# Kernel optimization log

Measured on AMD Instinct MI355X. Metric: run time of the kernel, lower is better.

Reference implementation:

```python
import jax, jax.numpy as jnp
import numpy as np

B, L, H, NH, NB = 8, 200, 128, 4, 2
HD = H // NH
ITEM_NUM, TIME_SPAN = 50000, 256
PAD = -2.0**32 + 1.0


def setup_inputs() -> dict:
    key = jax.random.key(0)
    ks = jax.random.split(key, 32)
    def g(i, shape, s=0.02):
        return jax.random.normal(ks[i], shape, jnp.float32) * s
    item_emb = g(0, (ITEM_NUM + 1, H)).at[0].set(0.0)  # padding_idx=0
    return dict(
        user_ids=jax.random.randint(ks[1], (B,), 0, 1000),
        log_seqs=jax.random.randint(ks[2], (B, L), 0, ITEM_NUM),
        time_matrices=jax.random.randint(ks[3], (B, L, L), 0, TIME_SPAN + 1),
        pos_seqs=jax.random.randint(ks[4], (B, L), 0, ITEM_NUM + 1),
        neg_seqs=jax.random.randint(ks[5], (B, L), 0, ITEM_NUM + 1),
        item_emb=item_emb,
        pos_K_emb=g(6, (L, H)), pos_V_emb=g(7, (L, H)),
        time_K_emb=g(8, (TIME_SPAN + 1, H)), time_V_emb=g(9, (TIME_SPAN + 1, H)),
        attn_ln_g=jnp.ones((NB, H)), attn_ln_b=jnp.zeros((NB, H)),
        Wq=g(10, (NB, H, H)), bq=jnp.zeros((NB, H)),
        Wk=g(11, (NB, H, H)), bk=jnp.zeros((NB, H)),
        Wv=g(12, (NB, H, H)), bv=jnp.zeros((NB, H)),
        fwd_ln_g=jnp.ones((NB, H)), fwd_ln_b=jnp.zeros((NB, H)),
        W1=g(13, (NB, H, H)), b1=jnp.zeros((NB, H)),
        W2=g(14, (NB, H, H)), b2=jnp.zeros((NB, H)),
        last_ln_g=jnp.ones((H,)), last_ln_b=jnp.zeros((H,)),
    )


def _ln(x, g, b, eps=1e-8):
    m = x.mean(-1, keepdims=True)
    v = jnp.var(x, axis=-1, keepdims=True)
    return (x - m) / jnp.sqrt(v + eps) * g + b


def _heads(x):
    # [..., H] -> [NH, ..., HD]; matches torch.cat(torch.split(x, HD, -1), 0)
    y = x.reshape(x.shape[:-1] + (NH, HD))
    return jnp.moveaxis(y, -2, 0)


def reference(user_ids, log_seqs, time_matrices, pos_seqs, neg_seqs, item_emb,
              pos_K_emb, pos_V_emb, time_K_emb, time_V_emb,
              attn_ln_g, attn_ln_b, Wq, bq, Wk, bk, Wv, bv,
              fwd_ln_g, fwd_ln_b, W1, b1, W2, b2, last_ln_g, last_ln_b):
    # user_ids is unused in the original forward as well.
    tmask = log_seqs == 0                                  # [B,L] True = pad
    keep = (~tmask)[..., None].astype(jnp.float32)
    seqs = item_emb[log_seqs] * np.float32(np.sqrt(H))
    seqs = seqs * keep
    pKh = _heads(pos_K_emb)                                # [NH,L,HD]
    pVh = _heads(pos_V_emb)
    tKh = _heads(time_K_emb[time_matrices])                # [NH,B,L,L,HD]
    tVh = _heads(time_V_emb[time_matrices])
    causal = ~jnp.tril(jnp.ones((L, L), bool))             # True above diag -> masked
    bad = tmask[:, :, None] | causal[None]                 # [B,L,L]
    scale = np.float32(np.sqrt(HD))
    for i in range(NB):
        Qin = _ln(seqs, attn_ln_g[i], attn_ln_b[i])
        Qh = _heads(Qin @ Wq[i].T + bq[i])                 # [NH,B,L,HD]
        Kh = _heads(seqs @ Wk[i].T + bk[i])
        Vh = _heads(seqs @ Wv[i].T + bv[i])
        attn = (jnp.einsum('nbqd,nbkd->nbqk', Qh, Kh)
                + jnp.einsum('nbqd,nkd->nbqk', Qh, pKh)
                + jnp.einsum('nbqkd,nbqd->nbqk', tKh, Qh)) / scale
        attn = jnp.where(bad[None], PAD, attn)
        attn = jax.nn.softmax(attn, axis=-1)
        out = (jnp.einsum('nbqk,nbkd->nbqd', attn, Vh)
               + jnp.einsum('nbqk,nkd->nbqd', attn, pVh)
               + jnp.einsum('nbqk,nbqkd->nbqd', attn, tVh))
        out = jnp.moveaxis(out, 0, -2).reshape(seqs.shape)  # merge heads -> [B,L,H]
        seqs = Qin + out                                    # residual uses LN'd Q (as in source)
        seqs = _ln(seqs, fwd_ln_g[i], fwd_ln_b[i])
        ff = jax.nn.relu(seqs @ W1[i].T + b1[i]) @ W2[i].T + b2[i] + seqs
        seqs = ff * keep
    log_feats = _ln(seqs, last_ln_g, last_ln_b)
    pos_logits = (log_feats * item_emb[pos_seqs]).sum(-1)   # [B,L]
    neg_logits = (log_feats * item_emb[neg_seqs]).sum(-1)
    return pos_logits, neg_logits
```

## Files before the change

kernel.cpp:

```cpp
#include <hip/hip_runtime.h>
#include <hip/hip_bf16.h>

#define BB 8
#define LL 200
#define HH 128
#define NHEAD 4
#define HDIM 32
#define NBLK 2
#define BL (BB * LL)
#define NT 257
#define QT 8
#define NQT 25
#define SSP 208
#define KC 132
#define ASP 36
#define BSP 66
#define FSP 132

static constexpr float SQRT_H    = 11.313708498984761f;
static constexpr float INV_SCALE = 0.17677669529663687f;
static constexpr float PADV      = -4294967295.0f;

__global__ void k_qkv_gemm(const float* __restrict__ seqs_in,
                           const int* __restrict__ log_seqs,
                           const float* __restrict__ item_emb,
                           const float* __restrict__ g, const float* __restrict__ bia,
                           const float* __restrict__ Wq, const float* __restrict__ bq,
                           const float* __restrict__ Wk, const float* __restrict__ bk,
                           const float* __restrict__ Wv, const float* __restrict__ bv,
                           const float* __restrict__ posK, const float* __restrict__ posV,
                           float* __restrict__ Qin, float* __restrict__ Q,
                           float* __restrict__ K, float* __restrict__ V) {
    int mt = blockIdx.x / 6, nt = blockIdx.x % 6;
    int matsel = nt >> 1;
    int jb = (nt & 1) * 64;
    int row0 = mt * 32;
    int tid = threadIdx.x;
    __shared__ float As[128 * ASP];
    __shared__ float Bs[128 * BSP];

    {
        int r = tid >> 3, seg = tid & 7;
        int row = row0 + r;
        float4 vv[4];
        if (seqs_in) {
            #pragma unroll
            for (int i = 0; i < 4; i++)
                vv[i] = *(const float4*)(seqs_in + (size_t)row * HH + seg * 16 + i * 4);
        } else {
            int idx = log_seqs[row];
            if (idx == 0) {
                #pragma unroll
                for (int i = 0; i < 4; i++) vv[i] = make_float4(0.f, 0.f, 0.f, 0.f);
            } else {
                #pragma unroll
                for (int i = 0; i < 4; i++) {
                    float4 e = *(const float4*)(item_emb + (size_t)idx * HH + seg * 16 + i * 4);
                    vv[i] = make_float4(e.x * SQRT_H, e.y * SQRT_H, e.z * SQRT_H, e.w * SQRT_H);
                }
            }
        }
        if (matsel == 0) {
            float s = 0.f, s2 = 0.f;
            #pragma unroll
            for (int i = 0; i < 4; i++) {
                s  += vv[i].x + vv[i].y + vv[i].z + vv[i].w;
                s2 += vv[i].x * vv[i].x + vv[i].y * vv[i].y + vv[i].z * vv[i].z + vv[i].w * vv[i].w;
            }
            #pragma unroll
            for (int off = 1; off < 8; off <<= 1) {
                s  += __shfl_xor(s, off);
                s2 += __shfl_xor(s2, off);
            }
            float mean = s * (1.f / HH);
            float var  = s2 * (1.f / HH) - mean * mean;
            float inv  = 1.f / sqrtf(var + 1e-8f);
            #pragma unroll
            for (int i = 0; i < 4; i++) {
                int k = seg * 16 + i * 4;
                float4 g4 = *(const float4*)(g + k);
                float4 b4 = *(const float4*)(bia + k);
                float4 y;
                y.x = (vv[i].x - mean) * inv * g4.x + b4.x;
                y.y = (vv[i].y - mean) * inv * g4.y + b4.y;
                y.z = (vv[i].z - mean) * inv * g4.z + b4.z;
                y.w = (vv[i].w - mean) * inv * g4.w + b4.w;
                As[(k + 0) * ASP + r] = y.x;
                As[(k + 1) * ASP + r] = y.y;
                As[(k + 2) * ASP + r] = y.z;
                As[(k + 3) * ASP + r] = y.w;
                if (nt == 0) *(float4*)(Qin + (size_t)row * HH + k) = y;
            }
        } else {
            #pragma unroll
            for (int i = 0; i < 4; i++) {
                int k = seg * 16 + i * 4;
                As[(k + 0) * ASP + r] = vv[i].x;
                As[(k + 1) * ASP + r] = vv[i].y;
                As[(k + 2) * ASP + r] = vv[i].z;
                As[(k + 3) * ASP + r] = vv[i].w;
            }
        }
    }
    {
        const float* W = (matsel == 0) ? Wq : (matsel == 1) ? Wk : Wv;
        int k4 = tid & 31, jj0 = tid >> 5;
        #pragma unroll
        for (int p = 0; p < 8; p++) {
            int jj = jj0 + p * 8;
            float4 w = *(const float4*)(W + (size_t)(jb + jj) * HH + k4 * 4);
            Bs[(k4 * 4 + 0) * BSP + jj] = w.x;
            Bs[(k4 * 4 + 1) * BSP + jj] = w.y;
            Bs[(k4 * 4 + 2) * BSP + jj] = w.z;
            Bs[(k4 * 4 + 3) * BSP + jj] = w.w;
        }
    }
    __syncthreads();

    int my = tid >> 5, jx = tid & 31;
    float a00=0,a01=0,a10=0,a11=0,a20=0,a21=0,a30=0,a31=0;
    #pragma unroll 4
    for (int k = 0; k < HH; k++) {
        float4 a = *(const float4*)&As[k * ASP + my * 4];
        float2 b = *(const float2*)&Bs[k * BSP + jx * 2];
        a00 += a.x * b.x; a01 += a.x * b.y;
        a10 += a.y * b.x; a11 += a.y * b.y;
        a20 += a.z * b.x; a21 += a.z * b.y;
        a30 += a.w * b.x; a31 += a.w * b.y;
    }
    float accs[4][2] = {{a00,a01},{a10,a11},{a20,a21},{a30,a31}};
    int col = jb + jx * 2;
    if (matsel == 0) {
        float2 bb = *(const float2*)(bq + col);
        #pragma unroll
        for (int r = 0; r < 4; r++) {
            int row = row0 + my * 4 + r;
            float2 o = make_float2((accs[r][0] + bb.x) * INV_SCALE,
                                   (accs[r][1] + bb.y) * INV_SCALE);
            *(float2*)(Q + (size_t)row * HH + col) = o;
        }
    } else if (matsel == 1) {
        float2 bb = *(const float2*)(bk + col);
        #pragma unroll
        for (int r = 0; r < 4; r++) {
            int row = row0 + my * 4 + r;
            int l = row % LL;
            float2 pk = *(const float2*)(posK + (size_t)l * HH + col);
            *(float2*)(K + (size_t)row * HH + col) =
                make_float2(accs[r][0] + bb.x + pk.x, accs[r][1] + bb.y + pk.y);
        }
    } else {
        float2 bb = *(const float2*)(bv + col);
        #pragma unroll
        for (int r = 0; r < 4; r++) {
            int row = row0 + my * 4 + r;
            int l = row % LL;
            float2 pv = *(const float2*)(posV + (size_t)l * HH + col);
            *(float2*)(V + (size_t)row * HH + col) =
                make_float2(accs[r][0] + bb.x + pv.x, accs[r][1] + bb.y + pv.y);
        }
    }
}

__global__ void k_attn(const float* __restrict__ Q, const float* __restrict__ K,
                       const float* __restrict__ V,
                       const float* __restrict__ timeK, const float* __restrict__ timeV,
                       const int* __restrict__ tm,
                       float* __restrict__ att) {
    int bn = blockIdx.x & 31;
    int b = bn >> 2, n = bn & 3;
    int qt = (NQT - 1) - (blockIdx.x >> 5);
    int q0 = qt * QT;
    int kmax = q0 + QT - 1;
    int tid = threadIdx.x;
    int wv = tid >> 6, ln = tid & 63;

    __shared__ float Qs[QT * HDIM];
    __shared__ float KstT[HDIM * KC];
    __shared__ float DTW[QT * NT];
    __shared__ float Ssc[QT * SSP];
    __shared__ unsigned short tmst[QT * LL];
    __shared__ float Ost[QT * HDIM];

    Ost[tid] = 0.f;
    if (tid < 64) {
        int qi = tid >> 3, d4 = tid & 7;
        *(float4*)(Qs + qi * HDIM + d4 * 4) =
            *(const float4*)(Q + ((size_t)(b * LL + q0 + qi)) * HH + n * HDIM + d4 * 4);
    }
    for (int idx = tid; idx < QT * LL; idx += 256) {
        int qi = idx / LL, k = idx - qi * LL;
        tmst[idx] = (unsigned short)tm[((size_t)(b * LL + q0 + qi)) * LL + k];
    }
    __syncthreads();

    int qi_c = tid >> 5, k2 = tid & 31;

    for (int c = 0; c < 2; c++) {
        int base = c * 128, rows = c ? 129 : 128;
        #pragma unroll
        for (int p = 0; p < 5; p++) {
            int idx = tid + p * 256;
            int r = idx >> 3, d4 = idx & 7;
            if (r < rows) {
                float4 w = *(const float4*)(timeK + (size_t)(base + r) * HH + n * HDIM + d4 * 4);
                KstT[(d4 * 4 + 0) * KC + r] = w.x;
                KstT[(d4 * 4 + 1) * KC + r] = w.y;
                KstT[(d4 * 4 + 2) * KC + r] = w.z;
                KstT[(d4 * 4 + 3) * KC + r] = w.w;
            }
        }
        __syncthreads();
        float a0 = 0, a1 = 0, a2 = 0, a3 = 0;
        int col = k2 * 4;
        #pragma unroll 8
        for (int d = 0; d < HDIM; d++) {
            float qv = Qs[qi_c * HDIM + d];
            float4 kv = *(const float4*)&KstT[d * KC + col];
            a0 += qv * kv.x; a1 += qv * kv.y; a2 += qv * kv.z; a3 += qv * kv.w;
        }
        float* dt = &DTW[qi_c * NT + base + col];
        dt[0] = a0; dt[1] = a1; dt[2] = a2; dt[3] = a3;
        if (c == 1 && k2 == 0) {
            float a = 0.f;
            #pragma unroll 8
            for (int d = 0; d < HDIM; d++) a += Qs[qi_c * HDIM + d] * KstT[d * KC + 128];
            DTW[qi_c * NT + 256] = a;
        }
        __syncthreads();
    }

    int nch = (kmax >> 7) + 1;
    for (int c = 0; c < nch; c++) {
        int base = c * 128;
        int rows = min(128, kmax + 1 - base);
        #pragma unroll
        for (int p = 0; p < 4; p++) {
            int idx = tid + p * 256;
            int r = idx >> 3, d4 = idx & 7;
            if (r < rows) {
                float4 w = *(const float4*)(K + ((size_t)(b * LL + base + r)) * HH + n * HDIM + d4 * 4);
                KstT[(d4 * 4 + 0) * KC + r] = w.x;
                KstT[(d4 * 4 + 1) * KC + r] = w.y;
                KstT[(d4 * 4 + 2) * KC + r] = w.z;
                KstT[(d4 * 4 + 3) * KC + r] = w.w;
            }
        }
        __syncthreads();
        float av[4] = {0, 0, 0, 0};
        int col = k2 * 4;
        #pragma unroll 8
        for (int d = 0; d < HDIM; d++) {
            float qv = Qs[qi_c * HDIM + d];
            float4 kv = *(const float4*)&KstT[d * KC + col];
            av[0] += qv * kv.x; av[1] += qv * kv.y; av[2] += qv * kv.z; av[3] += qv * kv.w;
        }
        int q = q0 + qi_c;
        #pragma unroll
        for (int j = 0; j < 4; j++) {
            int k = base + col + j;
            if (k <= q)
                Ssc[qi_c * SSP + k] = av[j] + DTW[qi_c * NT + tmst[qi_c * LL + k]];
        }
        __syncthreads();
    }

    for (int rr = 0; rr < 2; rr++) {
        int qi = wv + rr * 4;
        int q = q0 + qi;
        float sv[4];
        float m = -3.0e38f;
        #pragma unroll
        for (int jj = 0; jj < 4; jj++) {
            int k = ln + 64 * jj;
            sv[jj] = (k <= q) ? Ssc[qi * SSP + k] : -3.0e38f;
            m = fmaxf(m, sv[jj]);
        }
        for (int off = 32; off; off >>= 1) m = fmaxf(m, __shfl_xor(m, off));
        float sum = 0.f;
        #pragma unroll
        for (int jj = 0; jj < 4; jj++) {
            int k = ln + 64 * jj;
            sv[jj] = (k <= q) ? __expf(sv[jj] - m) : 0.f;
            sum += sv[jj];
        }
        for (int off = 32; off; off >>= 1) sum += __shfl_xor(sum, off);
        float inv = 1.f / sum;
        #pragma unroll
        for (int jj = 0; jj < 4; jj++) {
            int k = ln + 64 * jj;
            if (k <= q) Ssc[qi * SSP + k] = sv[jj] * inv;
        }
    }
    __syncthreads();

    int d = tid & 31, kg = tid >> 5;
    float acc[QT] = {0,0,0,0,0,0,0,0};
    const float* vb  = V + ((size_t)(b * LL)) * HH + n * HDIM + d;
    const float* tvb = timeV + n * HDIM + d;
    for (int k = kg; k <= kmax; k += 8) {
        float v = vb[(size_t)k * HH];
        #pragma unroll
        for (int qi = 0; qi < QT; qi++) {
            if (q0 + qi >= k) {
                float tv = tvb[(size_t)tmst[qi * LL + k] * HH];
                acc[qi] += Ssc[qi * SSP + k] * (v + tv);
            }
        }
    }
    #pragma unroll
    for (int qi = 0; qi < QT; qi++) {
        acc[qi] += __shfl_xor(acc[qi], 32);
        if ((kg & 1) == 0) atomicAdd(&Ost[qi * HDIM + d], acc[qi]);
    }
    __syncthreads();
    {
        int qi = tid >> 5;
        att[((size_t)(b * LL + q0 + qi)) * HH + n * HDIM + (tid & 31)] = Ost[tid];
    }
}

__global__ void k_ffn(const float* __restrict__ Qin, const float* __restrict__ att,
                      const float* __restrict__ g, const float* __restrict__ bia,
                      const float* __restrict__ W1, const float* __restrict__ b1,
                      const float* __restrict__ W2, const float* __restrict__ b2,
                      const int* __restrict__ log_seqs,
                      const float* __restrict__ lg, const float* __restrict__ lb,
                      const float* __restrict__ item_emb,
                      const int* __restrict__ pos, const int* __restrict__ neg,
                      float* __restrict__ out, float* __restrict__ logits, int last) {
    int row0 = blockIdx.x * 4;
    int tid = threadIdx.x;
    int wv = tid >> 6, ln = tid & 63;
    __shared__ float As[4 * FSP];
    __shared__ float H1[4 * FSP];
    __shared__ float Bs[128 * BSP];

    {
        int row = row0 + wv;
        float v0 = Qin[(size_t)row * HH + ln]      + att[(size_t)row * HH + ln];
        float v1 = Qin[(size_t)row * HH + ln + 64] + att[(size_t)row * HH + ln + 64];
        float s = v0 + v1, s2 = v0 * v0 + v1 * v1;
        for (int off = 32; off; off >>= 1) {
            s  += __shfl_xor(s, off);
            s2 += __shfl_xor(s2, off);
        }
        float mean = s * (1.f / HH);
        float var  = s2 * (1.f / HH) - mean * mean;
        float inv  = 1.f / sqrtf(var + 1e-8f);
        As[wv * FSP + ln]      = (v0 - mean) * inv * g[ln]      + bia[ln];
        As[wv * FSP + ln + 64] = (v1 - mean) * inv * g[ln + 64] + bia[ln + 64];
    }
    __syncthreads();

    int jx = ln;
    for (int c = 0; c < 2; c++) {
        int k4 = tid & 31, jj0 = tid >> 5;
        #pragma unroll
        for (int p = 0; p < 8; p++) {
            int jj = jj0 + p * 8;
            float4 w = *(const float4*)(W1 + (size_t)(c * 64 + jj) * HH + k4 * 4);
            Bs[(k4 * 4 + 0) * BSP + jj] = w.x;
            Bs[(k4 * 4 + 1) * BSP + jj] = w.y;
            Bs[(k4 * 4 + 2) * BSP + jj] = w.z;
            Bs[(k4 * 4 + 3) * BSP + jj] = w.w;
        }
        __syncthreads();
        float acc = 0.f;
        #pragma unroll 8
        for (int k = 0; k < HH; k++)
            acc += As[wv * FSP + k] * Bs[k * BSP + jx];
        int col = c * 64 + jx;
        float t = acc + b1[col];
        H1[wv * FSP + col] = t > 0.f ? t : 0.f;
        __syncthreads();
    }

    int rowm = row0 + wv;
    int keepz = (log_seqs[rowm] == 0);
    for (int c = 0; c < 2; c++) {
        int k4 = tid & 31, jj0 = tid >> 5;
        #pragma unroll
        for (int p = 0; p < 8; p++) {
            int jj = jj0 + p * 8;
            float4 w = *(const float4*)(W2 + (size_t)(c * 64 + jj) * HH + k4 * 4);
            Bs[(k4 * 4 + 0) * BSP + jj] = w.x;
            Bs[(k4 * 4 + 1) * BSP + jj] = w.y;
            Bs[(k4 * 4 + 2) * BSP + jj] = w.z;
            Bs[(k4 * 4 + 3) * BSP + jj] = w.w;
        }
        __syncthreads();
        float acc = 0.f;
        #pragma unroll 8
        for (int k = 0; k < HH; k++)
            acc += H1[wv * FSP + k] * Bs[k * BSP + jx];
        int col = c * 64 + jx;
        float o = acc + b2[col] + As[wv * FSP + col];
        if (keepz) o = 0.f;
        if (!last) out[(size_t)rowm * HH + col] = o;
        As[wv * FSP + col] = o;
        __syncthreads();
    }

    if (last) {
        float o0 = As[wv * FSP + ln], o1 = As[wv * FSP + ln + 64];
        float s = o0 + o1, s2 = o0 * o0 + o1 * o1;
        for (int off = 32; off; off >>= 1) {
            s  += __shfl_xor(s, off);
            s2 += __shfl_xor(s2, off);
        }
        float mean = s * (1.f / HH);
        float var  = s2 * (1.f / HH) - mean * mean;
        float inv  = 1.f / sqrtf(var + 1e-8f);
        float f0 = (o0 - mean) * inv * lg[ln]      + lb[ln];
        float f1 = (o1 - mean) * inv * lg[ln + 64] + lb[ln + 64];
        int ip = pos[rowm], in_ = neg[rowm];
        float vp = f0 * item_emb[(size_t)ip * HH + ln] + f1 * item_emb[(size_t)ip * HH + ln + 64];
        float vn = f0 * item_emb[(size_t)in_ * HH + ln] + f1 * item_emb[(size_t)in_ * HH + ln + 64];
        for (int off = 32; off; off >>= 1) {
            vp += __shfl_xor(vp, off);
            vn += __shfl_xor(vn, off);
        }
        if (ln == 0) {
            logits[rowm]      = vp;
            logits[BL + rowm] = vn;
        }
    }
}

extern "C" void kernel_launch(void* const* d_in, const int* in_sizes, int n_in,
                              void* d_out, int out_size, void* d_ws, size_t ws_size,
                              hipStream_t stream) {
    const int* log_seqs   = (const int*)d_in[1];
    const int* tm         = (const int*)d_in[2];
    const int* pos_seqs   = (const int*)d_in[3];
    const int* neg_seqs   = (const int*)d_in[4];
    const float* item_emb = (const float*)d_in[5];
    const float* posK     = (const float*)d_in[6];
    const float* posV     = (const float*)d_in[7];
    const float* timeK    = (const float*)d_in[8];
    const float* timeV    = (const float*)d_in[9];
    const float* attn_g   = (const float*)d_in[10];
    const float* attn_b   = (const float*)d_in[11];
    const float* Wq       = (const float*)d_in[12];
    const float* bq       = (const float*)d_in[13];
    const float* Wk       = (const float*)d_in[14];
    const float* bk       = (const float*)d_in[15];
    const float* Wv       = (const float*)d_in[16];
    const float* bv       = (const float*)d_in[17];
    const float* fwd_g    = (const float*)d_in[18];
    const float* fwd_b    = (const float*)d_in[19];
    const float* W1       = (const float*)d_in[20];
    const float* b1       = (const float*)d_in[21];
    const float* W2       = (const float*)d_in[22];
    const float* b2       = (const float*)d_in[23];
    const float* last_g   = (const float*)d_in[24];
    const float* last_b   = (const float*)d_in[25];

    float* seqs = (float*)d_ws;
    float* Qin  = seqs + (size_t)BL * HH;
    float* Qb   = Qin  + (size_t)BL * HH;
    float* Kb   = Qb   + (size_t)BL * HH;
    float* Vb   = Kb   + (size_t)BL * HH;
    float* att  = Vb   + (size_t)BL * HH;

    for (int i = 0; i < NBLK; i++) {
        k_qkv_gemm<<<300, 256, 0, stream>>>(i == 0 ? nullptr : seqs, log_seqs, item_emb,
                                            attn_g + i * HH, attn_b + i * HH,
                                            Wq + (size_t)i * HH * HH, bq + i * HH,
                                            Wk + (size_t)i * HH * HH, bk + i * HH,
                                            Wv + (size_t)i * HH * HH, bv + i * HH,
                                            posK, posV, Qin, Qb, Kb, Vb);
        k_attn<<<NQT * 32, 256, 0, stream>>>(Qb, Kb, Vb, timeK, timeV, tm, att);
        k_ffn<<<BL / 4, 256, 0, stream>>>(Qin, att, fwd_g + i * HH, fwd_b + i * HH,
                                          W1 + (size_t)i * HH * HH, b1 + i * HH,
                                          W2 + (size_t)i * HH * HH, b2 + i * HH,
                                          log_seqs, last_g, last_b, item_emb,
                                          pos_seqs, neg_seqs,
                                          seqs, (float*)d_out, (i == NBLK - 1) ? 1 : 0);
    }
}
```

Measured before the change: 258.2 us.

## Restructure attention: 4 queries per block, time-bucket weight histogram for timeV

```diff
diff --git a/kernel.cpp b/kernel.cpp
--- a/kernel.cpp
+++ b/kernel.cpp
@@ -9,17 +9,15 @@
 #define NBLK 2
 #define BL (BB * LL)
 #define NT 257
-#define QT 8
-#define NQT 25
+#define NQT4 50
 #define SSP 208
-#define KC 132
+#define KSP 36
 #define ASP 36
 #define BSP 66
 #define FSP 132
 
 static constexpr float SQRT_H    = 11.313708498984761f;
 static constexpr float INV_SCALE = 0.17677669529663687f;
-static constexpr float PADV      = -4294967295.0f;
 
 __global__ void k_qkv_gemm(const float* __restrict__ seqs_in,
                            const int* __restrict__ log_seqs,
@@ -135,9 +133,8 @@
         #pragma unroll
         for (int r = 0; r < 4; r++) {
             int row = row0 + my * 4 + r;
-            float2 o = make_float2((accs[r][0] + bb.x) * INV_SCALE,
-                                   (accs[r][1] + bb.y) * INV_SCALE);
-            *(float2*)(Q + (size_t)row * HH + col) = o;
+            *(float2*)(Q + (size_t)row * HH + col) =
+                make_float2((accs[r][0] + bb.x) * INV_SCALE, (accs[r][1] + bb.y) * INV_SCALE);
         }
     } else if (matsel == 1) {
         float2 bb = *(const float2*)(bk + col);
@@ -169,63 +166,60 @@
                        float* __restrict__ att) {
     int bn = blockIdx.x & 31;
     int b = bn >> 2, n = bn & 3;
-    int qt = (NQT - 1) - (blockIdx.x >> 5);
-    int q0 = qt * QT;
-    int kmax = q0 + QT - 1;
+    int qt = (NQT4 - 1) - (blockIdx.x >> 5);
+    int q0 = qt * 4;
+    int kmax = q0 + 3;
     int tid = threadIdx.x;
     int wv = tid >> 6, ln = tid & 63;
 
-    __shared__ float Qs[QT * HDIM];
-    __shared__ float KstT[HDIM * KC];
-    __shared__ float DTW[QT * NT];
-    __shared__ float Ssc[QT * SSP];
-    __shared__ unsigned short tmst[QT * LL];
-    __shared__ float Ost[QT * HDIM];
-
-    Ost[tid] = 0.f;
-    if (tid < 64) {
-        int qi = tid >> 3, d4 = tid & 7;
-        *(float4*)(Qs + qi * HDIM + d4 * 4) =
-            *(const float4*)(Q + ((size_t)(b * LL + q0 + qi)) * HH + n * HDIM + d4 * 4);
-    }
-    for (int idx = tid; idx < QT * LL; idx += 256) {
+    __shared__ float Kst[128 * KSP];
+    __shared__ float DTW[4 * NT];
+    __shared__ float WB[4 * NT];
+    __shared__ float Ssc[4 * SSP];
+    __shared__ int   tmst[4 * LL];
+    __shared__ float Qs[4][HDIM];
+    __shared__ float Ost[4 * HDIM];
+
+    if (tid < 128) {
+        int qi = tid >> 5, d = tid & 31;
+        Qs[qi][d] = Q[((size_t)(b * LL + q0 + qi)) * HH + n * HDIM + d];
+        Ost[tid] = 0.f;
+    }
+    for (int idx = tid; idx < 4 * NT; idx += 256) WB[idx] = 0.f;
+    for (int idx = tid; idx < 4 * LL; idx += 256) {
         int qi = idx / LL, k = idx - qi * LL;
-        tmst[idx] = (unsigned short)tm[((size_t)(b * LL + q0 + qi)) * LL + k];
+        tmst[idx] = tm[((size_t)(b * LL + q0 + qi)) * LL + k];
     }
     __syncthreads();
 
-    int qi_c = tid >> 5, k2 = tid & 31;
+    float qreg[HDIM];
+    #pragma unroll
+    for (int d = 0; d < HDIM; d++) qreg[d] = Qs[wv][d];
+    int q_my = q0 + wv;
 
     for (int c = 0; c < 2; c++) {
-        int base = c * 128, rows = c ? 129 : 128;
-        #pragma unroll
-        for (int p = 0; p < 5; p++) {
-            int idx = tid + p * 256;
+        int base = c * 128;
+        int rows = c ? (NT - 128) : 128;
+        int tot = rows * 8;
+        for (int idx = tid; idx < tot; idx += 256) {
             int r = idx >> 3, d4 = idx & 7;
-            if (r < rows) {
-                float4 w = *(const float4*)(timeK + (size_t)(base + r) * HH + n * HDIM + d4 * 4);
-                KstT[(d4 * 4 + 0) * KC + r] = w.x;
-                KstT[(d4 * 4 + 1) * KC + r] = w.y;
-                KstT[(d4 * 4 + 2) * KC + r] = w.z;
-                KstT[(d4 * 4 + 3) * KC + r] = w.w;
-            }
-        }
-        __syncthreads();
-        float a0 = 0, a1 = 0, a2 = 0, a3 = 0;
-        int col = k2 * 4;
-        #pragma unroll 8
-        for (int d = 0; d < HDIM; d++) {
-            float qv = Qs[qi_c * HDIM + d];
-            float4 kv = *(const float4*)&KstT[d * KC + col];
-            a0 += qv * kv.x; a1 += qv * kv.y; a2 += qv * kv.z; a3 += qv * kv.w;
-        }
-        float* dt = &DTW[qi_c * NT + base + col];
-        dt[0] = a0; dt[1] = a1; dt[2] = a2; dt[3] = a3;
-        if (c == 1 && k2 == 0) {
-            float a = 0.f;
-            #pragma unroll 8
-            for (int d = 0; d < HDIM; d++) a += Qs[qi_c * HDIM + d] * KstT[d * KC + 128];
-            DTW[qi_c * NT + 256] = a;
+            *(float4*)&Kst[r * KSP + d4 * 4] =
+                *(const float4*)(timeK + (size_t)(base + r) * HH + n * HDIM + d4 * 4);
+        }
+        __syncthreads();
+        #pragma unroll
+        for (int j = 0; j < 3; j++) {
+            int rl = ln + 64 * j;
+            if (rl < rows) {
+                float a = 0.f;
+                #pragma unroll
+                for (int d4 = 0; d4 < 8; d4++) {
+                    float4 kk = *(const float4*)&Kst[rl * KSP + d4 * 4];
+                    a += qreg[d4*4+0] * kk.x + qreg[d4*4+1] * kk.y
+                       + qreg[d4*4+2] * kk.z + qreg[d4*4+3] * kk.w;
+                }
+                DTW[wv * NT + base + rl] = a;
+            }
         }
         __syncthreads();
     }
@@ -234,89 +228,86 @@
     for (int c = 0; c < nch; c++) {
         int base = c * 128;
         int rows = min(128, kmax + 1 - base);
-        #pragma unroll
-        for (int p = 0; p < 4; p++) {
-            int idx = tid + p * 256;
+        int tot = rows * 8;
+        for (int idx = tid; idx < tot; idx += 256) {
             int r = idx >> 3, d4 = idx & 7;
-            if (r < rows) {
-                float4 w = *(const float4*)(K + ((size_t)(b * LL + base + r)) * HH + n * HDIM + d4 * 4);
-                KstT[(d4 * 4 + 0) * KC + r] = w.x;
-                KstT[(d4 * 4 + 1) * KC + r] = w.y;
-                KstT[(d4 * 4 + 2) * KC + r] = w.z;
-                KstT[(d4 * 4 + 3) * KC + r] = w.w;
-            }
-        }
-        __syncthreads();
-        float av[4] = {0, 0, 0, 0};
-        int col = k2 * 4;
-        #pragma unroll 8
-        for (int d = 0; d < HDIM; d++) {
-            float qv = Qs[qi_c * HDIM + d];
-            float4 kv = *(const float4*)&KstT[d * KC + col];
-            av[0] += qv * kv.x; av[1] += qv * kv.y; av[2] += qv * kv.z; av[3] += qv * kv.w;
-        }
-        int q = q0 + qi_c;
-        #pragma unroll
-        for (int j = 0; j < 4; j++) {
-            int k = base + col + j;
-            if (k <= q)
-                Ssc[qi_c * SSP + k] = av[j] + DTW[qi_c * NT + tmst[qi_c * LL + k]];
-        }
-        __syncthreads();
-    }
-
-    for (int rr = 0; rr < 2; rr++) {
-        int qi = wv + rr * 4;
-        int q = q0 + qi;
+            *(float4*)&Kst[r * KSP + d4 * 4] =
+                *(const float4*)(K + ((size_t)(b * LL + base + r)) * HH + n * HDIM + d4 * 4);
+        }
+        __syncthreads();
+        #pragma unroll
+        for (int j = 0; j < 2; j++) {
+            int rl = ln + 64 * j;
+            int k = base + rl;
+            if (rl < rows && k <= q_my) {
+                float a = 0.f;
+                #pragma unroll
+                for (int d4 = 0; d4 < 8; d4++) {
+                    float4 kk = *(const float4*)&Kst[rl * KSP + d4 * 4];
+                    a += qreg[d4*4+0] * kk.x + qreg[d4*4+1] * kk.y
+                       + qreg[d4*4+2] * kk.z + qreg[d4*4+3] * kk.w;
+                }
+                Ssc[wv * SSP + k] = a + DTW[wv * NT + tmst[wv * LL + k]];
+            }
+        }
+        __syncthreads();
+    }
+
+    {
         float sv[4];
         float m = -3.0e38f;
         #pragma unroll
-        for (int jj = 0; jj < 4; jj++) {
-            int k = ln + 64 * jj;
-            sv[jj] = (k <= q) ? Ssc[qi * SSP + k] : -3.0e38f;
-            m = fmaxf(m, sv[jj]);
+        for (int j = 0; j < 4; j++) {
+            int k = ln + 64 * j;
+            sv[j] = (k <= q_my) ? Ssc[wv * SSP + k] : -3.0e38f;
+            m = fmaxf(m, sv[j]);
         }
         for (int off = 32; off; off >>= 1) m = fmaxf(m, __shfl_xor(m, off));
         float sum = 0.f;
         #pragma unroll
-        for (int jj = 0; jj < 4; jj++) {
-            int k = ln + 64 * jj;
-            sv[jj] = (k <= q) ? __expf(sv[jj] - m) : 0.f;
-            sum += sv[jj];
+        for (int j = 0; j < 4; j++) {
+            int k = ln + 64 * j;
+            sv[j] = (k <= q_my) ? __expf(sv[j] - m) : 0.f;
+            sum += sv[j];
         }
         for (int off = 32; off; off >>= 1) sum += __shfl_xor(sum, off);
         float inv = 1.f / sum;
         #pragma unroll
-        for (int jj = 0; jj < 4; jj++) {
-            int k = ln + 64 * jj;
-            if (k <= q) Ssc[qi * SSP + k] = sv[jj] * inv;
+        for (int j = 0; j < 4; j++) {
+            int k = ln + 64 * j;
+            float p = sv[j] * inv;
+            if (k < SSP) Ssc[wv * SSP + k] = (k <= q_my) ? p : 0.f;
+            if (k <= q_my) atomicAdd(&WB[wv * NT + tmst[wv * LL + k]], p);
         }
     }
     __syncthreads();
 
     int d = tid & 31, kg = tid >> 5;
-    float acc[QT] = {0,0,0,0,0,0,0,0};
-    const float* vb  = V + ((size_t)(b * LL)) * HH + n * HDIM + d;
-    const float* tvb = timeV + n * HDIM + d;
+    float a0 = 0.f, a1 = 0.f, a2 = 0.f, a3 = 0.f;
+    const float* vb = V + ((size_t)(b * LL)) * HH + n * HDIM + d;
     for (int k = kg; k <= kmax; k += 8) {
         float v = vb[(size_t)k * HH];
-        #pragma unroll
-        for (int qi = 0; qi < QT; qi++) {
-            if (q0 + qi >= k) {
-                float tv = tvb[(size_t)tmst[qi * LL + k] * HH];
-                acc[qi] += Ssc[qi * SSP + k] * (v + tv);
-            }
-        }
-    }
-    #pragma unroll
-    for (int qi = 0; qi < QT; qi++) {
-        acc[qi] += __shfl_xor(acc[qi], 32);
-        if ((kg & 1) == 0) atomicAdd(&Ost[qi * HDIM + d], acc[qi]);
-    }
+        a0 += Ssc[0 * SSP + k] * v;
+        a1 += Ssc[1 * SSP + k] * v;
+        a2 += Ssc[2 * SSP + k] * v;
+        a3 += Ssc[3 * SSP + k] * v;
+    }
+    const float* tvb = timeV + n * HDIM + d;
+    for (int t = kg; t < NT; t += 8) {
+        float v = tvb[(size_t)t * HH];
+        a0 += WB[0 * NT + t] * v;
+        a1 += WB[1 * NT + t] * v;
+        a2 += WB[2 * NT + t] * v;
+        a3 += WB[3 * NT + t] * v;
+    }
+    atomicAdd(&Ost[0 * HDIM + d], a0);
+    atomicAdd(&Ost[1 * HDIM + d], a1);
+    atomicAdd(&Ost[2 * HDIM + d], a2);
+    atomicAdd(&Ost[3 * HDIM + d], a3);
     __syncthreads();
-    {
-        int qi = tid >> 5;
-        att[((size_t)(b * LL + q0 + qi)) * HH + n * HDIM + (tid & 31)] = Ost[tid];
+    if (tid < 128) {
+        int qi = tid >> 5, dd = tid & 31;
+        att[((size_t)(b * LL + q0 + qi)) * HH + n * HDIM + dd] = Ost[tid];
     }
 }
 
@@ -471,7 +462,7 @@
                                             Wk + (size_t)i * HH * HH, bk + i * HH,
                                             Wv + (size_t)i * HH * HH, bv + i * HH,
                                             posK, posV, Qin, Qb, Kb, Vb);
-        k_attn<<<NQT * 32, 256, 0, stream>>>(Qb, Kb, Vb, timeK, timeV, tm, att);
+        k_attn<<<NQT4 * 32, 256, 0, stream>>>(Qb, Kb, Vb, timeK, timeV, tm, att);
         k_ffn<<<BL / 4, 256, 0, stream>>>(Qin, att, fwd_g + i * HH, fwd_b + i * HH,
                                           W1 + (size_t)i * HH * HH, b1 + i * HH,
                                           W2 + (size_t)i * HH * HH, b2 + i * HH,
```

After: 249.6 us. 3.3% less time.
